# Optimization experiments

Hardware: AMD Instinct MI355X
Metric: run time of the kernel (lower is better)

The kernel has to match this reference:

```python
import jax, jax.numpy as jnp
import numpy as np

B, T, D, V, N = 64, 512, 256, 32000, 48


def gru_layer(x_tbd, wx, wh, b):
    """Keras GRU (reset_after=True). x_tbd: [T,B,Din]; returns [T,B,D]."""
    bx, bh = b[0], b[1]
    px = x_tbd @ wx + bx  # [T,B,3D] precomputed input projections
    units = wh.shape[0]

    def step(h, pxt):
        ph = h @ wh + bh
        xz, xr, xh = jnp.split(pxt, 3, axis=-1)
        hz, hr, hh = jnp.split(ph, 3, axis=-1)
        z = jax.nn.sigmoid(xz + hz)
        r = jax.nn.sigmoid(xr + hr)
        hc = jnp.tanh(xh + r * hh)
        hn = z * h + (1.0 - z) * hc
        return hn, hn

    h0 = jnp.zeros((x_tbd.shape[1], units), x_tbd.dtype)
    _, out = jax.lax.scan(step, h0, px)
    return out


def crf_log_likelihood(emis, tags, seq_len, trans):
    Bb, Tt, Nn = emis.shape
    t_idx = jnp.arange(Tt)
    mask = (t_idx[None, :] < seq_len[:, None]).astype(emis.dtype)  # [B,T]
    unary = jnp.take_along_axis(emis, tags[..., None], axis=2)[..., 0]
    us = jnp.sum(unary * mask, axis=1)
    tr = trans[tags[:, :-1], tags[:, 1:]]  # [B,T-1]
    ts = jnp.sum(tr * mask[:, 1:], axis=1)

    def step(alpha, inp):
        e_t, m_t = inp  # [B,N], [B]
        new = jax.nn.logsumexp(alpha[:, :, None] + trans[None], axis=1) + e_t
        return jnp.where(m_t[:, None], new, alpha), None

    alpha, _ = jax.lax.scan(step, emis[:, 0],
                            (emis.transpose(1, 0, 2)[1:], (mask > 0).T[1:]))
    log_z = jax.nn.logsumexp(alpha, axis=-1)
    return us + ts - log_z


def crf_decode(emis, trans, seq_len):
    Bb, Tt, Nn = emis.shape
    mask = jnp.arange(Tt)[None, :] < seq_len[:, None]
    ident = jnp.arange(Nn, dtype=jnp.int32)[None, :]

    def step(alpha, inp):
        e_t, m_t = inp
        sc = alpha[:, :, None] + trans[None]  # [B,N,N] prev->cur
        bp = jnp.argmax(sc, axis=1).astype(jnp.int32)
        new = jnp.max(sc, axis=1) + e_t
        alpha_n = jnp.where(m_t[:, None], new, alpha)
        bp = jnp.where(m_t[:, None], bp, ident)
        return alpha_n, bp

    alpha, bps = jax.lax.scan(step, emis[:, 0],
                              (emis.transpose(1, 0, 2)[1:], mask.T[1:]))
    score = jnp.max(alpha, axis=-1)
    last = jnp.argmax(alpha, axis=-1).astype(jnp.int32)  # [B]

    def back(tag, bp):
        prev = jnp.take_along_axis(bp, tag[:, None], axis=1)[:, 0]
        return prev, tag

    tag0, tags = jax.lax.scan(back, last, bps, reverse=True)  # tags[i]=pos i+1
    pred = jnp.concatenate([tag0[:, None], tags.T], axis=1)  # [B,T]
    return pred, score


def setup_inputs() -> dict:
    key = jax.random.key(0)
    ks = jax.random.split(key, 20)
    s = 0.05
    inp = {
        'x': jax.random.randint(ks[0], (B, T), 0, V, dtype=jnp.int32),
        'y': jax.random.randint(ks[1], (B, T), 0, N, dtype=jnp.int32),
        'seq_len': jax.random.randint(ks[2], (B,), T // 2, T + 1, dtype=jnp.int32),
        'embed': jax.random.normal(ks[3], (V, D), jnp.float32) * s,
        'wx_f': jax.random.normal(ks[4], (D, 3 * D), jnp.float32) * s,
        'wh_f': jax.random.normal(ks[5], (D, 3 * D), jnp.float32) * s,
        'b_f': jnp.zeros((2, 3 * D), jnp.float32),
        'wx_b': jax.random.normal(ks[6], (D, 3 * D), jnp.float32) * s,
        'wh_b': jax.random.normal(ks[7], (D, 3 * D), jnp.float32) * s,
        'b_b': jnp.zeros((2, 3 * D), jnp.float32),
        'wq': jax.random.normal(ks[8], (2 * D, D), jnp.float32) * s,
        'bq': jnp.zeros((D,), jnp.float32),
        'wk': jax.random.normal(ks[9], (2 * D, D), jnp.float32) * s,
        'bk': jnp.zeros((D,), jnp.float32),
        'wv': jax.random.normal(ks[10], (2 * D, D), jnp.float32) * s,
        'bv': jnp.zeros((D,), jnp.float32),
        'wt': jax.random.normal(ks[11], (D, N), jnp.float32) * s,
        'bt': jnp.zeros((N,), jnp.float32),
        'trans': jax.random.normal(ks[12], (N, N), jnp.float32) * s,
    }
    return inp


def reference(x, y, seq_len, embed, wx_f, wh_f, b_f, wx_b, wh_b, b_b,
              wq, bq, wk, bk, wv, bv, wt, bt, trans):
    emb = embed[x]  # [B,T,D]
    xt = emb.transpose(1, 0, 2)  # [T,B,D]
    hf = gru_layer(xt, wx_f, wh_f, b_f)
    hb = gru_layer(xt[::-1], wx_b, wh_b, b_b)[::-1]
    h = jnp.concatenate([hf, hb], axis=-1).transpose(1, 0, 2)  # [B,T,2D]
    q = h @ wq + bq
    k = h @ wk + bk
    v = h @ wv + bv
    w = jax.nn.softmax(jnp.einsum('btd,bsd->bts', q, k), axis=-1)
    a = jnp.einsum('bts,bsd->btd', w, v)
    logits = a @ wt + bt  # [B,T,N]
    pred, _ = crf_decode(logits, trans, seq_len)
    ll = crf_log_likelihood(logits, y, seq_len, trans)
    return pred, ll
```

## Files before the change

kernel.cpp:

```cpp
#include <hip/hip_runtime.h>
#include <math.h>

typedef float f32;
typedef short short8 __attribute__((ext_vector_type(8)));
typedef float f32x4 __attribute__((ext_vector_type(4)));

#define TT 512
#define BB 64
#define DD 256
#define NN 48

static const size_t OFF_EBF  = 0;
static const size_t OFF_PXF  = 16384000;
static const size_t OFF_PXB  = OFF_PXF + 50331648;
static const size_t OFF_HBF_F= OFF_PXB + 50331648;
static const size_t OFF_HBF_B= OFF_HBF_F + 16777216;
static const size_t OFF_WXTF = OFF_HBF_B + 16777216;
static const size_t OFF_WXTB = OFF_WXTF + 393216;
static const size_t OFF_WHTF = OFF_WXTB + 393216;
static const size_t OFF_WHTB = OFF_WHTF + 393216;
static const size_t OFF_WQT  = OFF_WHTB + 393216;
static const size_t OFF_WKT  = OFF_WQT + 262144;
static const size_t OFF_WVT  = OFF_WKT + 262144;
static const size_t OFF_WTT  = OFF_WVT + 262144;
static const size_t OFF_QBF = OFF_PXF;
static const size_t OFF_KBF = OFF_QBF + 16777216;
static const size_t OFF_VBF = OFF_KBF + 16777216;
static const size_t OFF_VT  = OFF_VBF + 16777216;
static const size_t OFF_SCB = OFF_VT  + 16777216;
static const size_t OFF_ABF = OFF_QBF;
static const size_t OFF_LG  = OFF_KBF;

__device__ __forceinline__ ushort f2bf(f32 f) {
  union { f32 f; unsigned u; } v; v.f = f;
  unsigned r = v.u + 0x7fffu + ((v.u >> 16) & 1u);
  return (ushort)(r >> 16);
}
__device__ __forceinline__ f32 bf2f(ushort u) {
  union { unsigned u; f32 f; } v; v.u = ((unsigned)u) << 16; return v.f;
}
__device__ __forceinline__ f32 fsigmoid(f32 x) { return 1.f / (1.f + __expf(-x)); }
__device__ __forceinline__ f32 ftanh(f32 x) { return 1.f - 2.f / (__expf(2.f * x) + 1.f); }

template <int PL2>
__global__ __launch_bounds__(256) void tconv_k(
    const f32* __restrict__ in, ushort* __restrict__ out, int total, int Q) {
  int o = blockIdx.x * 256 + threadIdx.x;
  if (o >= total) return;
  int q = o >> PL2, p = o & ((1 << PL2) - 1);
  out[o] = f2bf(in[(size_t)p * Q + q]);
}

__global__ __launch_bounds__(256) void conv_embed_k(
    const f32* __restrict__ in, ushort* __restrict__ out, int n4) {
  int i = blockIdx.x * 256 + threadIdx.x;
  if (i >= n4) return;
  float4 v = ((const float4*)in)[i];
  ushort4 o;
  o.x = f2bf(v.x); o.y = f2bf(v.y); o.z = f2bf(v.z); o.w = f2bf(v.w);
  ((ushort4*)out)[i] = o;
}

__global__ __launch_bounds__(256) void tr_v_k(
    const ushort* __restrict__ in, ushort* __restrict__ out) {
  __shared__ ushort tile[32][33];
  int b = blockIdx.z;
  int s0 = blockIdx.x * 32, d0 = blockIdx.y * 32;
  int xc = threadIdx.x & 31, y0 = threadIdx.x >> 5;
  for (int yy = y0; yy < 32; yy += 8)
    tile[yy][xc] = in[((size_t)b * 512 + s0 + yy) * 256 + d0 + xc];
  __syncthreads();
  for (int yy = y0; yy < 32; yy += 8)
    out[((size_t)b * 256 + d0 + yy) * 512 + s0 + xc] = tile[xc][yy];
}

enum { GM_PX = 0, GM_QKV = 1, GM_SC = 2, GM_AV = 3, GM_LG = 4 };

template <int MODE>
__global__ __launch_bounds__(256) void mgemm(
    const ushort* __restrict__ Aa, const ushort* __restrict__ Ab,
    const ushort* __restrict__ Bt,
    f32* __restrict__ Cf, ushort* __restrict__ Cb,
    const f32* __restrict__ bias, const int* __restrict__ xi,
    int Ndim, int K, int rev) {
  const int m0 = blockIdx.y * 128;
  const int n0 = blockIdx.x * 128;
  const int bz = blockIdx.z;
  const int tid = threadIdx.x;
  const int l = tid & 63, w = tid >> 6;
  const int wr = w >> 1, wc = w & 1;
  __shared__ __align__(16) short Al[128 * 40];
  __shared__ __align__(16) short Bl[128 * 40];
  f32x4 acc[4][4] = {};

  const int rowa = tid >> 1;
  const int kha = (tid & 1) * 16;
  const int rA = m0 + rowa;
  const ushort* aBase = nullptr;
  const ushort* aBase2 = nullptr;
  if constexpr (MODE == GM_PX) {
    int tg = rA >> 6, b = rA & 63;
    int ts = rev ? (511 - tg) : tg;
    aBase = Aa + (size_t)xi[b * 512 + ts] * 256;
  } else if constexpr (MODE == GM_QKV) {
    int bl = rA >> 9, t = rA & 511;
    aBase = Aa + ((size_t)(t * 64 + bl)) * 256;
    aBase2 = Ab + ((size_t)((511 - t) * 64 + bl)) * 256;
  } else if constexpr (MODE == GM_SC) {
    aBase = Aa + ((size_t)(bz * 512 + rA)) * 256;
  } else if constexpr (MODE == GM_AV) {
    aBase = Aa + ((size_t)(bz * 512 + rA)) * 512;
  } else {
    aBase = Aa + (size_t)rA * 256;
  }
  const int rowb = tid >> 1;
  const int khb = (tid & 1) * 16;
  int rowg = n0 + rowb;
  if constexpr (MODE == GM_SC) rowg += bz * 512;
  if constexpr (MODE == GM_AV) rowg += bz * 256;
  const ushort* bBase = Bt + (size_t)rowg * K;
  const bool bValid = (MODE != GM_LG) || (n0 + rowb < Ndim);

  for (int k0 = 0; k0 < K; k0 += 32) {
    {
      int kk = k0 + kha;
      const ushort* src;
      if constexpr (MODE == GM_QKV)
        src = (kk < 256) ? aBase + kk : aBase2 + (kk - 256);
      else
        src = aBase + kk;
      uint4 a0 = *(const uint4*)src;
      uint4 a1 = *(const uint4*)(src + 8);
      *(uint4*)&Al[rowa * 40 + kha] = a0;
      *(uint4*)&Al[rowa * 40 + kha + 8] = a1;
    }
    {
      uint4 v0 = make_uint4(0, 0, 0, 0), v1 = make_uint4(0, 0, 0, 0);
      if (bValid) {
        const ushort* src = bBase + k0 + khb;
        v0 = *(const uint4*)src;
        v1 = *(const uint4*)(src + 8);
      }
      *(uint4*)&Bl[rowb * 40 + khb] = v0;
      *(uint4*)&Bl[rowb * 40 + khb + 8] = v1;
    }
    __syncthreads();
    const int fr = l & 15, fg = l >> 4;
    short8 af[4], bfr[4];
#pragma unroll
    for (int mf = 0; mf < 4; ++mf)
      af[mf] = *(const short8*)&Al[(wr * 64 + mf * 16 + fr) * 40 + fg * 8];
#pragma unroll
    for (int nf = 0; nf < 4; ++nf)
      bfr[nf] = *(const short8*)&Bl[(wc * 64 + nf * 16 + fr) * 40 + fg * 8];
#pragma unroll
    for (int mf = 0; mf < 4; ++mf)
#pragma unroll
      for (int nf = 0; nf < 4; ++nf)
        acc[mf][nf] = __builtin_amdgcn_mfma_f32_16x16x32_bf16(
            af[mf], bfr[nf], acc[mf][nf], 0, 0, 0);
    __syncthreads();
  }

  const int fr = l & 15, fq = l >> 4;
#pragma unroll
  for (int mf = 0; mf < 4; ++mf) {
#pragma unroll
    for (int nf = 0; nf < 4; ++nf) {
      int col = n0 + wc * 64 + nf * 16 + fr;
      f32 bs = 0.f;
      if (bias && col < Ndim) bs = bias[col];
#pragma unroll
      for (int rg = 0; rg < 4; ++rg) {
        int row = m0 + wr * 64 + mf * 16 + fq * 4 + rg;
        f32 vv = acc[mf][nf][rg] + bs;
        if constexpr (MODE == GM_PX)
          Cb[(size_t)row * 768 + col] = f2bf(vv);
        else if constexpr (MODE == GM_QKV)
          Cb[(size_t)row * 256 + col] = f2bf(vv);
        else if constexpr (MODE == GM_SC)
          Cb[((size_t)bz * 512 + row) * 512 + col] = f2bf(vv);
        else if constexpr (MODE == GM_AV)
          Cb[((size_t)bz * 512 + row) * 256 + col] = f2bf(vv);
        else {
          if (col < Ndim) Cf[(size_t)row * 48 + col] = vv;
        }
      }
    }
  }
}

__global__ __launch_bounds__(512, 1) void gru_scan4(
    const ushort* __restrict__ pxf, const ushort* __restrict__ pxb,
    const ushort* __restrict__ whtf, const ushort* __restrict__ whtb,
    const f32* __restrict__ b_f, const f32* __restrict__ b_b,
    ushort* __restrict__ hfbf, ushort* __restrict__ hbbf) {
  const int dir = blockIdx.x >> 2;
  const int rg4 = blockIdx.x & 3;
  const int tid = threadIdx.x;
  const int w = tid >> 6, l = tid & 63;
  const int fr = l & 15, fq = l >> 4;
  const ushort* px  = dir ? pxb : pxf;
  const ushort* wht = dir ? whtb : whtf;
  const f32* bh = (dir ? b_b : b_f) + 768;
  ushort* hseq = dir ? hbbf : hfbf;

  __shared__ __align__(16) char ldsWh[131072];
  __shared__ __align__(16) char ldsH[8192];

#pragma unroll
  for (int i = 0; i < 16; ++i) {
    int idx = i * 512 + tid;
    int col = idx >> 5, kc = idx & 31;
    uint4 v = *(const uint4*)&wht[(size_t)(512 + col) * 256 + kc * 8];
    *(uint4*)&ldsWh[col * 512 + ((kc * 16) ^ ((col & 7) << 4))] = v;
  }
  for (int i = tid; i < 512; i += 512) ((uint4*)ldsH)[i] = make_uint4(0, 0, 0, 0);

  const int ctb = w * 2;
  short8 wzv[2][8], wrv[2][8];
#pragma unroll
  for (int ct = 0; ct < 2; ++ct) {
    int col = (ctb + ct) * 16 + fr;
#pragma unroll
    for (int ks = 0; ks < 8; ++ks) {
      wzv[ct][ks] = *(const short8*)&wht[(size_t)col * 256 + ks * 32 + fq * 8];
      wrv[ct][ks] = *(const short8*)&wht[(size_t)(256 + col) * 256 + ks * 32 + fq * 8];
    }
  }
  f32 bhz[2], bhr[2], bhh[2];
#pragma unroll
  for (int ct = 0; ct < 2; ++ct) {
    int col = (ctb + ct) * 16 + fr;
    bhz[ct] = bh[col]; bhr[ct] = bh[256 + col]; bhh[ct] = bh[512 + col];
  }
  f32 hold[8];
#pragma unroll
  for (int i = 0; i < 8; ++i) hold[i] = 0.f;
  __syncthreads();

#pragma unroll 1
  for (int t = 0; t < TT; ++t) {
    ushort pz[8], pr_[8], ph[8];
    {
      const ushort* pxt = px + ((size_t)t * 64 + rg4 * 16) * 768;
#pragma unroll
      for (int ct = 0; ct < 2; ++ct) {
        int col = (ctb + ct) * 16 + fr;
#pragma unroll
        for (int ri = 0; ri < 4; ++ri) {
          const ushort* p = pxt + (fq * 4 + ri) * 768 + col;
          pz[ct * 4 + ri] = p[0];
          pr_[ct * 4 + ri] = p[256];
          ph[ct * 4 + ri] = p[512];
        }
      }
    }
    f32x4 az[2] = {}, ar[2] = {}, ah[2] = {};
#pragma unroll
    for (int ks = 0; ks < 8; ++ks) {
      short8 a = *(const short8*)&ldsH[fr * 512 + ((ks * 64 + fq * 16) ^ ((fr & 7) << 4))];
#pragma unroll
      for (int ct = 0; ct < 2; ++ct) {
        int col = (ctb + ct) * 16 + fr;
        az[ct] = __builtin_amdgcn_mfma_f32_16x16x32_bf16(a, wzv[ct][ks], az[ct], 0, 0, 0);
        ar[ct] = __builtin_amdgcn_mfma_f32_16x16x32_bf16(a, wrv[ct][ks], ar[ct], 0, 0, 0);
        short8 wh8 = *(const short8*)&ldsWh[col * 512 + ((ks * 64 + fq * 16) ^ ((col & 7) << 4))];
        ah[ct] = __builtin_amdgcn_mfma_f32_16x16x32_bf16(a, wh8, ah[ct], 0, 0, 0);
      }
    }
    ushort hnb[8];
#pragma unroll
    for (int ct = 0; ct < 2; ++ct)
#pragma unroll
      for (int ri = 0; ri < 4; ++ri) {
        int idx = ct * 4 + ri;
        f32 zv = fsigmoid(az[ct][ri] + bhz[ct] + bf2f(pz[idx]));
        f32 rv = fsigmoid(ar[ct][ri] + bhr[ct] + bf2f(pr_[idx]));
        f32 hc = ftanh(bf2f(ph[idx]) + rv * (ah[ct][ri] + bhh[ct]));
        f32 hn = zv * hold[idx] + (1.f - zv) * hc;
        hold[idx] = hn;
        hnb[idx] = f2bf(hn);
      }
    __syncthreads();
#pragma unroll
    for (int ct = 0; ct < 2; ++ct)
#pragma unroll
      for (int ri = 0; ri < 4; ++ri) {
        int col = (ctb + ct) * 16 + fr;
        int r = fq * 4 + ri;
        *(ushort*)&ldsH[r * 512 + ((col * 2) ^ ((r & 7) << 4))] = hnb[ct * 4 + ri];
      }
    __syncthreads();
    {
      int r = tid >> 5, kc = tid & 31;
      uint4 v = *(const uint4*)&ldsH[r * 512 + ((kc * 16) ^ ((r & 7) << 4))];
      *(uint4*)&hseq[((size_t)t * 64 + rg4 * 16 + r) * 256 + kc * 8] = v;
    }
  }
}

__global__ __launch_bounds__(256) void softmax_ip(ushort* __restrict__ p) {
  size_t row = blockIdx.x;
  uint* pr = (uint*)(p + row * 512);
  int tid = threadIdx.x;
  uint u = pr[tid];
  f32 v0 = bf2f((ushort)(u & 0xffff)), v1 = bf2f((ushort)(u >> 16));
  f32 m = fmaxf(v0, v1);
  for (int off = 32; off; off >>= 1) m = fmaxf(m, __shfl_xor(m, off));
  __shared__ f32 red[4];
  __shared__ f32 red2[4];
  if ((tid & 63) == 0) red[tid >> 6] = m;
  __syncthreads();
  m = fmaxf(fmaxf(red[0], red[1]), fmaxf(red[2], red[3]));
  f32 e0 = __expf(v0 - m), e1 = __expf(v1 - m);
  f32 s = e0 + e1;
  for (int off = 32; off; off >>= 1) s += __shfl_xor(s, off);
  if ((tid & 63) == 0) red2[tid >> 6] = s;
  __syncthreads();
  s = red2[0] + red2[1] + red2[2] + red2[3];
  f32 inv = 1.f / s;
  pr[tid] = (uint)f2bf(e0 * inv) | ((uint)f2bf(e1 * inv) << 16);
}

__global__ __launch_bounds__(64) void crf_ll_k(
    const f32* __restrict__ logits, const int* __restrict__ y,
    const int* __restrict__ seq_len, const f32* __restrict__ trans,
    f32* __restrict__ out) {
  const int b = blockIdx.x, tid = threadIdx.x;
  __shared__ f32 tr[NN][NN];
  __shared__ f32 al[2][NN];
  for (int i = tid; i < NN * NN; i += 64) tr[i / NN][i % NN] = trans[i];
  const f32* em = logits + (size_t)b * TT * NN;
  const int L = seq_len[b];
  if (tid < NN) al[0][tid] = em[tid];
  __syncthreads();
  int cur = 0;
  for (int t = 1; t < TT; ++t) {
    if (t >= L) break;
    if (tid < NN) {
      f32 m = -1e30f;
      for (int i = 0; i < NN; ++i) m = fmaxf(m, al[cur][i] + tr[i][tid]);
      f32 s = 0.f;
      for (int i = 0; i < NN; ++i) s += __expf(al[cur][i] + tr[i][tid] - m);
      al[cur ^ 1][tid] = m + __logf(s) + em[t * NN + tid];
    }
    __syncthreads();
    cur ^= 1;
  }
  f32 us = 0.f, ts = 0.f;
  for (int t = tid; t < TT; t += 64) {
    if (t < L) {
      us += em[t * NN + y[b * TT + t]];
      if (t >= 1) ts += tr[y[b * TT + t - 1]][y[b * TT + t]];
    }
  }
  for (int off = 32; off; off >>= 1) { us += __shfl_xor(us, off); ts += __shfl_xor(ts, off); }
  if (tid == 0) {
    f32 m = -1e30f;
    for (int i = 0; i < NN; ++i) m = fmaxf(m, al[cur][i]);
    f32 s = 0.f;
    for (int i = 0; i < NN; ++i) s += __expf(al[cur][i] - m);
    out[(size_t)BB * TT + b] = us + ts - (m + __logf(s));
  }
}

__global__ __launch_bounds__(64) void crf_decode_k(
    const f32* __restrict__ logits, const int* __restrict__ seq_len,
    const f32* __restrict__ trans, f32* __restrict__ out) {
  const int b = blockIdx.x, tid = threadIdx.x;
  __shared__ f32 tr[NN][NN];
  __shared__ f32 al[2][NN];
  __shared__ unsigned char bp[TT - 1][NN];
  __shared__ unsigned char pr[TT];
  for (int i = tid; i < NN * NN; i += 64) tr[i / NN][i % NN] = trans[i];
  const f32* em = logits + (size_t)b * TT * NN;
  const int L = seq_len[b];
  if (tid < NN) al[0][tid] = em[tid];
  __syncthreads();
  int cur = 0;
  for (int t = 1; t < TT; ++t) {
    if (tid < NN) {
      if (t < L) {
        f32 m = -1e30f; int arg = 0;
        for (int i = 0; i < NN; ++i) {
          f32 v = al[cur][i] + tr[i][tid];
          if (v > m) { m = v; arg = i; }
        }
        al[cur ^ 1][tid] = m + em[t * NN + tid];
        bp[t - 1][tid] = (unsigned char)arg;
      } else {
        al[cur ^ 1][tid] = al[cur][tid];
        bp[t - 1][tid] = (unsigned char)tid;
      }
    }
    __syncthreads();
    cur ^= 1;
  }
  if (tid == 0) {
    f32 m = -1e30f; int last = 0;
    for (int i = 0; i < NN; ++i)
      if (al[cur][i] > m) { m = al[cur][i]; last = i; }
    int tag = last;
    for (int t = TT - 2; t >= 0; --t) { pr[t + 1] = (unsigned char)tag; tag = bp[t][tag]; }
    pr[0] = (unsigned char)tag;
  }
  __syncthreads();
  for (int t = tid; t < TT; t += 64)
    out[(size_t)b * TT + t] = (f32)pr[t];
}

extern "C" void kernel_launch(void* const* d_in, const int* in_sizes, int n_in,
                              void* d_out, int out_size, void* d_ws, size_t ws_size,
                              hipStream_t stream) {
  const int* x       = (const int*)d_in[0];
  const int* y       = (const int*)d_in[1];
  const int* seq_len = (const int*)d_in[2];
  const f32* embed   = (const f32*)d_in[3];
  const f32* wx_f    = (const f32*)d_in[4];
  const f32* wh_f    = (const f32*)d_in[5];
  const f32* b_f     = (const f32*)d_in[6];
  const f32* wx_b    = (const f32*)d_in[7];
  const f32* wh_b    = (const f32*)d_in[8];
  const f32* b_b     = (const f32*)d_in[9];
  const f32* wq      = (const f32*)d_in[10];
  const f32* bq      = (const f32*)d_in[11];
  const f32* wk      = (const f32*)d_in[12];
  const f32* bk      = (const f32*)d_in[13];
  const f32* wv      = (const f32*)d_in[14];
  const f32* bv      = (const f32*)d_in[15];
  const f32* wt      = (const f32*)d_in[16];
  const f32* bt      = (const f32*)d_in[17];
  const f32* trans   = (const f32*)d_in[18];
  f32* out = (f32*)d_out;

  char* ws = (char*)d_ws;
  ushort* ebf  = (ushort*)(ws + OFF_EBF);
  ushort* pxfb = (ushort*)(ws + OFF_PXF);
  ushort* pxbb = (ushort*)(ws + OFF_PXB);
  ushort* hfbf = (ushort*)(ws + OFF_HBF_F);
  ushort* hbbf = (ushort*)(ws + OFF_HBF_B);
  ushort* wxtf = (ushort*)(ws + OFF_WXTF);
  ushort* wxtb = (ushort*)(ws + OFF_WXTB);
  ushort* whtf = (ushort*)(ws + OFF_WHTF);
  ushort* whtb = (ushort*)(ws + OFF_WHTB);
  ushort* wqt  = (ushort*)(ws + OFF_WQT);
  ushort* wkt  = (ushort*)(ws + OFF_WKT);
  ushort* wvt  = (ushort*)(ws + OFF_WVT);
  ushort* wtt  = (ushort*)(ws + OFF_WTT);
  ushort* qbf = (ushort*)(ws + OFF_QBF);
  ushort* kbf = (ushort*)(ws + OFF_KBF);
  ushort* vbf = (ushort*)(ws + OFF_VBF);
  ushort* vT  = (ushort*)(ws + OFF_VT);
  ushort* scb = (ushort*)(ws + OFF_SCB);
  ushort* abf = (ushort*)(ws + OFF_ABF);
  f32*    lg  = (f32*)(ws + OFF_LG);

  conv_embed_k<<<8000, 256, 0, stream>>>(embed, ebf, 2048000);
  tconv_k<8><<<768, 256, 0, stream>>>(wx_f, wxtf, 196608, 768);
  tconv_k<8><<<768, 256, 0, stream>>>(wx_b, wxtb, 196608, 768);
  tconv_k<8><<<768, 256, 0, stream>>>(wh_f, whtf, 196608, 768);
  tconv_k<8><<<768, 256, 0, stream>>>(wh_b, whtb, 196608, 768);
  tconv_k<9><<<512, 256, 0, stream>>>(wq, wqt, 131072, 256);
  tconv_k<9><<<512, 256, 0, stream>>>(wk, wkt, 131072, 256);
  tconv_k<9><<<512, 256, 0, stream>>>(wv, wvt, 131072, 256);
  tconv_k<8><<<48, 256, 0, stream>>>(wt, wtt, 12288, 48);

  mgemm<GM_PX><<<dim3(6, 256), 256, 0, stream>>>(
      ebf, nullptr, wxtf, nullptr, pxfb, b_f, x, 768, 256, 0);
  mgemm<GM_PX><<<dim3(6, 256), 256, 0, stream>>>(
      ebf, nullptr, wxtb, nullptr, pxbb, b_b, x, 768, 256, 1);
  gru_scan4<<<8, 512, 0, stream>>>(pxfb, pxbb, whtf, whtb, b_f, b_b, hfbf, hbbf);

  mgemm<GM_QKV><<<dim3(2, 256), 256, 0, stream>>>(
      hfbf, hbbf, wqt, nullptr, qbf, bq, nullptr, 256, 512, 0);
  mgemm<GM_QKV><<<dim3(2, 256), 256, 0, stream>>>(
      hfbf, hbbf, wkt, nullptr, kbf, bk, nullptr, 256, 512, 0);
  mgemm<GM_QKV><<<dim3(2, 256), 256, 0, stream>>>(
      hfbf, hbbf, wvt, nullptr, vbf, bv, nullptr, 256, 512, 0);
  tr_v_k<<<dim3(16, 8, 64), 256, 0, stream>>>(vbf, vT);
  mgemm<GM_SC><<<dim3(4, 4, 64), 256, 0, stream>>>(
      qbf, nullptr, kbf, nullptr, scb, nullptr, nullptr, 512, 256, 0);
  softmax_ip<<<BB * TT, 256, 0, stream>>>(scb);
  mgemm<GM_AV><<<dim3(2, 4, 64), 256, 0, stream>>>(
      scb, nullptr, vT, nullptr, abf, nullptr, nullptr, 256, 512, 0);
  mgemm<GM_LG><<<dim3(1, 256), 256, 0, stream>>>(
      abf, nullptr, wtt, lg, nullptr, bt, nullptr, 48, 256, 0);

  crf_ll_k<<<BB, 64, 0, stream>>>(lg, y, seq_len, trans, out);
  crf_decode_k<<<BB, 64, 0, stream>>>(lg, seq_len, trans, out);
}
```

Baseline: 2.903 ms.

## Double-buffer GRU hidden state, prefetch projections, register-based CRF forward

The GRU scan now keeps two LDS hidden-state buffers, so each step needs one barrier instead of two. It also prefetches the next timestep's input projections into registers while the current step computes, and writes the previous step's hidden output early in the step. The CRF log-likelihood kernel moves to a wavefront-only forward pass: it holds exp(trans) columns in registers and uses shuffles for the max and the sum, which removes per-step LDS traffic and barriers. The cost is higher register pressure in both kernels, and the CRF pass now computes sum(exp(alpha-m)*exp(trans)) rather than a per-column max, which is a numerics change.

```diff
diff --git a/kernel.cpp b/kernel.cpp
--- a/kernel.cpp
+++ b/kernel.cpp
@@ -190,7 +190,7 @@
   }
 }
 
-__global__ __launch_bounds__(512, 1) void gru_scan4(
+__global__ __launch_bounds__(512, 1) void gru_scan5(
     const ushort* __restrict__ pxf, const ushort* __restrict__ pxb,
     const ushort* __restrict__ whtf, const ushort* __restrict__ whtb,
     const f32* __restrict__ b_f, const f32* __restrict__ b_b,
@@ -206,7 +206,7 @@
   ushort* hseq = dir ? hbbf : hfbf;
 
   __shared__ __align__(16) char ldsWh[131072];
-  __shared__ __align__(16) char ldsH[8192];
+  __shared__ __align__(16) char ldsH[2][8192];
 
 #pragma unroll
   for (int i = 0; i < 16; ++i) {
@@ -215,7 +215,7 @@
     uint4 v = *(const uint4*)&wht[(size_t)(512 + col) * 256 + kc * 8];
     *(uint4*)&ldsWh[col * 512 + ((kc * 16) ^ ((col & 7) << 4))] = v;
   }
-  for (int i = tid; i < 512; i += 512) ((uint4*)ldsH)[i] = make_uint4(0, 0, 0, 0);
+  ((uint4*)ldsH[0])[tid] = make_uint4(0, 0, 0, 0);
 
   const int ctb = w * 2;
   short8 wzv[2][8], wrv[2][8];
@@ -237,29 +237,33 @@
   f32 hold[8];
 #pragma unroll
   for (int i = 0; i < 8; ++i) hold[i] = 0.f;
-  __syncthreads();
-
-#pragma unroll 1
-  for (int t = 0; t < TT; ++t) {
-    ushort pz[8], pr_[8], ph[8];
-    {
-      const ushort* pxt = px + ((size_t)t * 64 + rg4 * 16) * 768;
-#pragma unroll
-      for (int ct = 0; ct < 2; ++ct) {
-        int col = (ctb + ct) * 16 + fr;
-#pragma unroll
-        for (int ri = 0; ri < 4; ++ri) {
-          const ushort* p = pxt + (fq * 4 + ri) * 768 + col;
-          pz[ct * 4 + ri] = p[0];
-          pr_[ct * 4 + ri] = p[256];
-          ph[ct * 4 + ri] = p[512];
-        }
-      }
+
+  auto loadpx = [&](int t, ushort* pv) {
+    const ushort* pxt = px + ((size_t)t * 64 + rg4 * 16) * 768;
+#pragma unroll
+    for (int ct = 0; ct < 2; ++ct) {
+      int col = (ctb + ct) * 16 + fr;
+#pragma unroll
+      for (int ri = 0; ri < 4; ++ri) {
+        const ushort* p = pxt + (fq * 4 + ri) * 768 + col;
+        pv[(ct * 4 + ri) * 3 + 0] = p[0];
+        pv[(ct * 4 + ri) * 3 + 1] = p[256];
+        pv[(ct * 4 + ri) * 3 + 2] = p[512];
+      }
+    }
+  };
+
+  auto step = [&](int t, int buf, const ushort* pc, ushort* pn) {
+    if (t + 1 < TT) loadpx(t + 1, pn);
+    if (t > 0) {
+      int r = tid >> 5, kc = tid & 31;
+      uint4 v = *(const uint4*)&ldsH[buf][r * 512 + ((kc * 16) ^ ((r & 7) << 4))];
+      *(uint4*)&hseq[((size_t)(t - 1) * 64 + rg4 * 16 + r) * 256 + kc * 8] = v;
     }
     f32x4 az[2] = {}, ar[2] = {}, ah[2] = {};
 #pragma unroll
     for (int ks = 0; ks < 8; ++ks) {
-      short8 a = *(const short8*)&ldsH[fr * 512 + ((ks * 64 + fq * 16) ^ ((fr & 7) << 4))];
+      short8 a = *(const short8*)&ldsH[buf][fr * 512 + ((ks * 64 + fq * 16) ^ ((fr & 7) << 4))];
 #pragma unroll
       for (int ct = 0; ct < 2; ++ct) {
         int col = (ctb + ct) * 16 + fr;
@@ -269,34 +273,35 @@
         ah[ct] = __builtin_amdgcn_mfma_f32_16x16x32_bf16(a, wh8, ah[ct], 0, 0, 0);
       }
     }
-    ushort hnb[8];
 #pragma unroll
     for (int ct = 0; ct < 2; ++ct)
 #pragma unroll
       for (int ri = 0; ri < 4; ++ri) {
         int idx = ct * 4 + ri;
-        f32 zv = fsigmoid(az[ct][ri] + bhz[ct] + bf2f(pz[idx]));
-        f32 rv = fsigmoid(ar[ct][ri] + bhr[ct] + bf2f(pr_[idx]));
-        f32 hc = ftanh(bf2f(ph[idx]) + rv * (ah[ct][ri] + bhh[ct]));
+        f32 zv = fsigmoid(az[ct][ri] + bhz[ct] + bf2f(pc[idx * 3 + 0]));
+        f32 rv = fsigmoid(ar[ct][ri] + bhr[ct] + bf2f(pc[idx * 3 + 1]));
+        f32 hc = ftanh(bf2f(pc[idx * 3 + 2]) + rv * (ah[ct][ri] + bhh[ct]));
         f32 hn = zv * hold[idx] + (1.f - zv) * hc;
         hold[idx] = hn;
-        hnb[idx] = f2bf(hn);
-      }
-    __syncthreads();
-#pragma unroll
-    for (int ct = 0; ct < 2; ++ct)
-#pragma unroll
-      for (int ri = 0; ri < 4; ++ri) {
         int col = (ctb + ct) * 16 + fr;
         int r = fq * 4 + ri;
-        *(ushort*)&ldsH[r * 512 + ((col * 2) ^ ((r & 7) << 4))] = hnb[ct * 4 + ri];
+        *(ushort*)&ldsH[buf ^ 1][r * 512 + ((col * 2) ^ ((r & 7) << 4))] = f2bf(hn);
       }
     __syncthreads();
-    {
-      int r = tid >> 5, kc = tid & 31;
-      uint4 v = *(const uint4*)&ldsH[r * 512 + ((kc * 16) ^ ((r & 7) << 4))];
-      *(uint4*)&hseq[((size_t)t * 64 + rg4 * 16 + r) * 256 + kc * 8] = v;
-    }
+  };
+
+  ushort pA[24], pB[24];
+  loadpx(0, pA);
+  __syncthreads();
+#pragma unroll 1
+  for (int t2 = 0; t2 < TT; t2 += 2) {
+    step(t2, 0, pA, pB);
+    step(t2 + 1, 1, pB, pA);
+  }
+  {
+    int r = tid >> 5, kc = tid & 31;
+    uint4 v = *(const uint4*)&ldsH[0][r * 512 + ((kc * 16) ^ ((r & 7) << 4))];
+    *(uint4*)&hseq[((size_t)511 * 64 + rg4 * 16 + r) * 256 + kc * 8] = v;
   }
 }
 
@@ -328,41 +333,40 @@
     const int* __restrict__ seq_len, const f32* __restrict__ trans,
     f32* __restrict__ out) {
   const int b = blockIdx.x, tid = threadIdx.x;
-  __shared__ f32 tr[NN][NN];
-  __shared__ f32 al[2][NN];
-  for (int i = tid; i < NN * NN; i += 64) tr[i / NN][i % NN] = trans[i];
+  __shared__ f32 tr[NN * NN];
+  for (int i = tid; i < NN * NN; i += 64) tr[i] = trans[i];
   const f32* em = logits + (size_t)b * TT * NN;
   const int L = seq_len[b];
-  if (tid < NN) al[0][tid] = em[tid];
-  __syncthreads();
-  int cur = 0;
-  for (int t = 1; t < TT; ++t) {
-    if (t >= L) break;
-    if (tid < NN) {
-      f32 m = -1e30f;
-      for (int i = 0; i < NN; ++i) m = fmaxf(m, al[cur][i] + tr[i][tid]);
-      f32 s = 0.f;
-      for (int i = 0; i < NN; ++i) s += __expf(al[cur][i] + tr[i][tid] - m);
-      al[cur ^ 1][tid] = m + __logf(s) + em[t * NN + tid];
-    }
-    __syncthreads();
-    cur ^= 1;
+  const bool act = tid < NN;
+  f32 Ecol[NN];
+#pragma unroll
+  for (int i = 0; i < NN; ++i)
+    Ecol[i] = act ? __expf(trans[i * NN + tid]) : 0.f;
+  f32 alpha = act ? em[tid] : -1e30f;
+  __syncthreads();
+  for (int t = 1; t < L; ++t) {
+    f32 m = alpha;
+    for (int off = 32; off; off >>= 1) m = fmaxf(m, __shfl_xor(m, off));
+    f32 e = __expf(alpha - m);
+    f32 s = 0.f;
+#pragma unroll
+    for (int i = 0; i < NN; ++i) s += __shfl(e, i) * Ecol[i];
+    if (act) alpha = m + __logf(s) + em[t * NN + tid];
   }
   f32 us = 0.f, ts = 0.f;
   for (int t = tid; t < TT; t += 64) {
     if (t < L) {
       us += em[t * NN + y[b * TT + t]];
-      if (t >= 1) ts += tr[y[b * TT + t - 1]][y[b * TT + t]];
+      if (t >= 1) ts += tr[y[b * TT + t - 1] * NN + y[b * TT + t]];
     }
   }
   for (int off = 32; off; off >>= 1) { us += __shfl_xor(us, off); ts += __shfl_xor(ts, off); }
-  if (tid == 0) {
-    f32 m = -1e30f;
-    for (int i = 0; i < NN; ++i) m = fmaxf(m, al[cur][i]);
-    f32 s = 0.f;
-    for (int i = 0; i < NN; ++i) s += __expf(al[cur][i] - m);
-    out[(size_t)BB * TT + b] = us + ts - (m + __logf(s));
-  }
+  f32 m = alpha;
+  for (int off = 32; off; off >>= 1) m = fmaxf(m, __shfl_xor(m, off));
+  f32 e = __expf(alpha - m);
+  f32 s = e;
+  for (int off = 32; off; off >>= 1) s += __shfl_xor(s, off);
+  if (tid == 0) out[(size_t)BB * TT + b] = us + ts - (m + __logf(s));
 }
 
 __global__ __launch_bounds__(64) void crf_decode_k(
@@ -470,7 +474,7 @@
       ebf, nullptr, wxtf, nullptr, pxfb, b_f, x, 768, 256, 0);
   mgemm<GM_PX><<<dim3(6, 256), 256, 0, stream>>>(
       ebf, nullptr, wxtb, nullptr, pxbb, b_b, x, 768, 256, 1);
-  gru_scan4<<<8, 512, 0, stream>>>(pxfb, pxbb, whtf, whtb, b_f, b_b, hfbf, hbbf);
+  gru_scan5<<<8, 512, 0, stream>>>(pxfb, pxbb, whtf, whtb, b_f, b_b, hfbf, hbbf);
 
   mgemm<GM_QKV><<<dim3(2, 256), 256, 0, stream>>>(
       hfbf, hbbf, wqt, nullptr, qbf, bq, nullptr, 256, 512, 0);
```

Result: faster. 2.542 ms (-12.4%).
